# Optimization experiments

Measured on AMD Instinct MI355X. Metric: run time of the kernel, lower is better.

Reference implementation:

```python
import jax, jax.numpy as jnp
import numpy as np

N_NODES = 50000
N_EDGES = 800000
HIDDEN = 128


def setup_inputs() -> dict:
    key = jax.random.key(0)
    k_emb, k_ei, k1, k2, k3, kb1, kb2, kb3 = jax.random.split(key, 8)
    emb = jax.random.normal(k_emb, (N_NODES, HIDDEN), dtype=jnp.float32)
    edge_index = jax.random.randint(k_ei, (2, N_EDGES), 0, N_NODES, dtype=jnp.int64)
    h = HIDDEN
    # MLP([2h, 4h, h, 1]) weights, Kaiming-uniform-ish init
    def lin(k, fan_in, fan_out):
        bound = 1.0 / np.sqrt(fan_in)
        return jax.random.uniform(k, (fan_in, fan_out), jnp.float32, -bound, bound)
    W1 = lin(k1, 2 * h, 4 * h)
    b1 = jax.random.uniform(kb1, (4 * h,), jnp.float32, -1.0 / np.sqrt(2 * h), 1.0 / np.sqrt(2 * h))
    W2 = lin(k2, 4 * h, h)
    b2 = jax.random.uniform(kb2, (h,), jnp.float32, -1.0 / np.sqrt(4 * h), 1.0 / np.sqrt(4 * h))
    W3 = lin(k3, h, 1)
    b3 = jax.random.uniform(kb3, (1,), jnp.float32, -1.0 / np.sqrt(h), 1.0 / np.sqrt(h))
    return {"emb": emb, "edge_index": edge_index,
            "W1": W1, "b1": b1, "W2": W2, "b2": b2, "W3": W3, "b3": b3}


def reference(emb, edge_index, W1, b1, W2, b2, W3, b3):
    # learn_edge_att=True path: gather endpoints, concat, 3-layer MLP
    col, row = edge_index[0], edge_index[1]
    f12 = jnp.concatenate([emb[col], emb[row]], axis=-1)  # [E, 2h]
    x = jax.nn.relu(f12 @ W1 + b1)                         # [E, 4h]
    x = jax.nn.relu(x @ W2 + b2)                           # [E, h]
    att_log_logits = x @ W3 + b3                           # [E, 1]
    return att_log_logits
```

## Files before the change

kernel.cpp:

```cpp
#include <hip/hip_runtime.h>
#include <hip/hip_bf16.h>
#include <stdint.h>

#define N_EDGES   800000
#define N_NODESC  50000
#define HID       128

typedef __attribute__((ext_vector_type(8))) short bf16x8;
typedef __attribute__((ext_vector_type(4))) float f32x4;
typedef __attribute__((ext_vector_type(4))) unsigned int u32x4;

__device__ __forceinline__ short f2bf(float f) {
    union { float f; uint32_t u; } v; v.f = f;
    uint32_t r = v.u + 0x7FFFu + ((v.u >> 16) & 1u);
    return (short)(r >> 16);
}

__device__ __forceinline__ uint32_t packbf2(float lo, float hi) {
    float2 t; t.x = lo; t.y = hi;
    __hip_bfloat162 h = __float22bfloat162_rn(t);
    uint32_t u;
    __builtin_memcpy(&u, &h, 4);
    return u;
}

__device__ __forceinline__ uint32_t addrelu2(uint32_t a, uint32_t b) {
    __hip_bfloat162 ha, hb;
    __builtin_memcpy(&ha, &a, 4);
    __builtin_memcpy(&hb, &b, 4);
    __hip_bfloat162 s = __hadd2(ha, hb);
    uint32_t x;
    __builtin_memcpy(&x, &s, 4);
    uint32_t neg = (x & 0x80008000u) >> 15;
    return x & ~(neg * 0xFFFFu);
}
__device__ __forceinline__ bf16x8 addrelu8(u32x4 p, u32x4 q) {
    u32x4 r;
    #pragma unroll
    for (int j = 0; j < 4; ++j) r[j] = addrelu2(p[j], q[j]);
    bf16x8 out;
    __builtin_memcpy(&out, &r, 16);
    return out;
}

#define PQ_OFF   0UL
#define W1S_OFF  102400000UL
#define W2S_OFF  (W1S_OFF + 262144UL)

__global__ __launch_bounds__(256) void swizzle_kernel(const float* __restrict__ W1,
                                                      const float* __restrict__ W2,
                                                      short* __restrict__ W1s,
                                                      short* __restrict__ W2s) {
    int t = blockIdx.x * 256 + threadIdx.x;
    int lane = t & 63;
    int kq = lane >> 4;
    int nn = lane & 15;
    if (t < 16384) {
        int frag = t >> 6;
        int kc = frag >> 6;
        int nt = frag & 63;
        int n = nt * 16 + nn;
        int kbase = kc * 32 + kq * 8;
        bf16x8 v;
        #pragma unroll
        for (int j = 0; j < 8; ++j) {
            int k = kbase + j;
            float f = (n < 512) ? W1[k * 512 + n] : W1[(128 + k) * 512 + (n - 512)];
            v[j] = f2bf(f);
        }
        *(bf16x8*)(W1s + frag * 512 + lane * 8) = v;
    } else if (t < 24576) {
        int t2 = t - 16384;
        int frag = t2 >> 6;
        int kc = frag >> 3;
        int nt = frag & 7;
        int n = nt * 16 + nn;
        int kbase = kc * 32 + kq * 8;
        bf16x8 v;
        #pragma unroll
        for (int j = 0; j < 8; ++j) v[j] = f2bf(W2[(kbase + j) * HID + n]);
        *(bf16x8*)(W2s + frag * 512 + lane * 8) = v;
    }
}

__global__ __launch_bounds__(256) void precompute_kernel(const float* __restrict__ emb,
                                                         const short* __restrict__ W1s,
                                                         const float* __restrict__ b1,
                                                         short* __restrict__ PQ) {
    int lane = threadIdx.x & 63;
    int w = threadIdx.x >> 6;
    int nb = blockIdx.x * 32;
    int m = lane & 15;
    int kq = lane >> 4;

    int n0 = nb + m;       if (n0 > N_NODESC - 1) n0 = N_NODESC - 1;
    int n1 = nb + 16 + m;  if (n1 > N_NODESC - 1) n1 = N_NODESC - 1;
    const float* a0p = emb + (size_t)n0 * 128 + kq * 8;
    const float* a1p = emb + (size_t)n1 * 128 + kq * 8;

    f32x4 acc[2][16];
    #pragma unroll
    for (int mt = 0; mt < 2; ++mt)
        #pragma unroll
        for (int i = 0; i < 16; ++i) acc[mt][i] = (f32x4){0.f, 0.f, 0.f, 0.f};

    #pragma unroll
    for (int kc = 0; kc < 4; ++kc) {
        f32x4 x0 = *(const f32x4*)(a0p + kc * 32);
        f32x4 x1 = *(const f32x4*)(a0p + kc * 32 + 4);
        f32x4 y0 = *(const f32x4*)(a1p + kc * 32);
        f32x4 y1 = *(const f32x4*)(a1p + kc * 32 + 4);
        u32x4 au, bu;
        au[0] = packbf2(x0[0], x0[1]); au[1] = packbf2(x0[2], x0[3]);
        au[2] = packbf2(x1[0], x1[1]); au[3] = packbf2(x1[2], x1[3]);
        bu[0] = packbf2(y0[0], y0[1]); bu[1] = packbf2(y0[2], y0[3]);
        bu[2] = packbf2(y1[0], y1[1]); bu[3] = packbf2(y1[2], y1[3]);
        bf16x8 a0, a1;
        __builtin_memcpy(&a0, &au, 16);
        __builtin_memcpy(&a1, &bu, 16);
        #pragma unroll
        for (int nt = 0; nt < 16; ++nt) {
            int frag = kc * 64 + (w * 16 + nt);
            bf16x8 b = *(const bf16x8*)(W1s + frag * 512 + lane * 8);
            acc[0][nt] = __builtin_amdgcn_mfma_f32_16x16x32_bf16(a0, b, acc[0][nt], 0, 0, 0);
            acc[1][nt] = __builtin_amdgcn_mfma_f32_16x16x32_bf16(a1, b, acc[1][nt], 0, 0, 0);
        }
    }

    #pragma unroll
    for (int nt = 0; nt < 16; ++nt) {
        int n = w * 256 + nt * 16 + m;
        float bias = (n < 512) ? b1[n] : 0.0f;
        #pragma unroll
        for (int mt = 0; mt < 2; ++mt) {
            #pragma unroll
            for (int r = 0; r < 4; ++r) {
                int node = nb + mt * 16 + kq * 4 + r;
                if (node < N_NODESC)
                    PQ[(size_t)node * 1024 + n] = f2bf(acc[mt][nt][r] + bias);
            }
        }
    }
}

__global__ __launch_bounds__(256, 2) void edge_kernel(const short* __restrict__ PQ,
                                                      const int* __restrict__ ei,
                                                      const short* __restrict__ W2s,
                                                      const float* __restrict__ b2,
                                                      const float* __restrict__ W3,
                                                      const float* __restrict__ b3,
                                                      float* __restrict__ out) {
    int lane = threadIdx.x & 63;
    int w = threadIdx.x >> 6;
    int e0 = blockIdx.x * 256 + w * 64;
    int m = lane & 15;
    int kq = lane >> 4;

    int idx_c = ei[e0 + lane];
    int idx_r = ei[N_EDGES + e0 + lane];

    const short* pb[4];
    const short* qb[4];
    #pragma unroll
    for (int t = 0; t < 4; ++t) {
        int ce = __shfl(idx_c, t * 16 + m, 64);
        int re = __shfl(idx_r, t * 16 + m, 64);
        pb[t] = PQ + (size_t)ce * 1024 + kq * 8;
        qb[t] = PQ + (size_t)re * 1024 + 512 + kq * 8;
    }

    f32x4 acc[4][8];
    #pragma unroll
    for (int t = 0; t < 4; ++t)
        #pragma unroll
        for (int nt = 0; nt < 8; ++nt) acc[t][nt] = (f32x4){0.f, 0.f, 0.f, 0.f};

    #pragma unroll
    for (int kc = 0; kc < 16; ++kc) {
        u32x4 p[4], q[4];
        #pragma unroll
        for (int t = 0; t < 4; ++t) {
            p[t] = *(const u32x4*)(pb[t] + kc * 32);
            q[t] = *(const u32x4*)(qb[t] + kc * 32);
        }
        bf16x8 b[8];
        #pragma unroll
        for (int nt = 0; nt < 8; ++nt)
            b[nt] = *(const bf16x8*)(W2s + (kc * 8 + nt) * 512 + lane * 8);
        #pragma unroll
        for (int t = 0; t < 4; ++t) {
            bf16x8 a = addrelu8(p[t], q[t]);
            #pragma unroll
            for (int nt = 0; nt < 8; ++nt)
                acc[t][nt] = __builtin_amdgcn_mfma_f32_16x16x32_bf16(a, b[nt], acc[t][nt], 0, 0, 0);
        }
    }

    float b2v[8], w3v[8];
    #pragma unroll
    for (int nt = 0; nt < 8; ++nt) {
        b2v[nt] = b2[nt * 16 + m];
        w3v[nt] = W3[nt * 16 + m];
    }
    float b3s = b3[0];
    #pragma unroll
    for (int t = 0; t < 4; ++t) {
        float partial[4] = {0.f, 0.f, 0.f, 0.f};
        #pragma unroll
        for (int nt = 0; nt < 8; ++nt) {
            #pragma unroll
            for (int r = 0; r < 4; ++r) {
                float x2 = acc[t][nt][r] + b2v[nt];
                x2 = x2 > 0.f ? x2 : 0.f;
                partial[r] += x2 * w3v[nt];
            }
        }
        #pragma unroll
        for (int r = 0; r < 4; ++r) {
            #pragma unroll
            for (int off = 1; off < 16; off <<= 1)
                partial[r] += __shfl_xor(partial[r], off, 64);
            if (m == 0) out[e0 + t * 16 + kq * 4 + r] = partial[r] + b3s;
        }
    }
}

extern "C" void kernel_launch(void* const* d_in, const int* in_sizes, int n_in,
                              void* d_out, int out_size, void* d_ws, size_t ws_size,
                              hipStream_t stream) {
    const float* emb = (const float*)d_in[0];
    const int*   ei  = (const int*)d_in[1];
    const float* W1  = (const float*)d_in[2];
    const float* b1  = (const float*)d_in[3];
    const float* W2  = (const float*)d_in[4];
    const float* b2  = (const float*)d_in[5];
    const float* W3  = (const float*)d_in[6];
    const float* b3  = (const float*)d_in[7];
    float* out = (float*)d_out;

    short* PQ  = (short*)((char*)d_ws + PQ_OFF);
    short* W1s = (short*)((char*)d_ws + W1S_OFF);
    short* W2s = (short*)((char*)d_ws + W2S_OFF);

    swizzle_kernel<<<96, 256, 0, stream>>>(W1, W2, W1s, W2s);
    precompute_kernel<<<(N_NODESC + 31) / 32, 256, 0, stream>>>(emb, W1s, b1, PQ);
    edge_kernel<<<N_EDGES / 256, 256, 0, stream>>>(PQ, ei, W2s, b2, W3, b3, out);
}
```

Measured before the change: 475.5 us.

## Counting-sort edges by source node and coalesce precompute stores via LDS

Adds a histogram, scan and scatter pass that sorts edges by their first endpoint, so the edge kernel reads PQ rows with better cache locality and writes outputs through a permutation index. The precompute kernel now stages results in shared memory and writes 16-byte coalesced rows instead of scattered 2-byte stores. The cost is four extra launches, atomics, a single-block serial scan, and scattered output writes.

Measured after the change: 555.5 us. +16.8%, slower.

```diff
diff --git a/kernel.cpp b/kernel.cpp
--- a/kernel.cpp
+++ b/kernel.cpp
@@ -43,9 +43,14 @@
     return out;
 }
 
-#define PQ_OFF   0UL
-#define W1S_OFF  102400000UL
-#define W2S_OFF  (W1S_OFF + 262144UL)
+#define PQ_OFF    0UL
+#define W1S_OFF   102400000UL
+#define W2S_OFF   (W1S_OFF + 262144UL)
+#define CNT_OFF   (W2S_OFF + 131072UL)
+#define CUR_OFF   (CNT_OFF + 200000UL)
+#define COLS_OFF  (CUR_OFF + 200000UL)
+#define ROWS_OFF  (COLS_OFF + 3200000UL)
+#define ES_OFF    (ROWS_OFF + 3200000UL)
 
 __global__ __launch_bounds__(256) void swizzle_kernel(const float* __restrict__ W1,
                                                       const float* __restrict__ W2,
@@ -83,10 +88,48 @@
     }
 }
 
+__global__ __launch_bounds__(256) void hist_kernel(const int* __restrict__ ei,
+                                                   int* __restrict__ cnt) {
+    int e = blockIdx.x * 256 + threadIdx.x;
+    atomicAdd(&cnt[ei[e]], 1);
+}
+
+__global__ __launch_bounds__(1024) void scan_kernel(const int* __restrict__ cnt,
+                                                    int* __restrict__ cursor) {
+    __shared__ int psum[1024];
+    int tid = threadIdx.x;
+    int lo = tid * 49;
+    int hi = lo + 49; if (hi > N_NODESC) hi = N_NODESC;
+    int s = 0;
+    for (int i = lo; i < hi; ++i) s += cnt[i];
+    psum[tid] = s;
+    __syncthreads();
+    if (tid == 0) {
+        int acc = 0;
+        for (int i = 0; i < 1024; ++i) { int t = psum[i]; psum[i] = acc; acc += t; }
+    }
+    __syncthreads();
+    int run = psum[tid];
+    for (int i = lo; i < hi; ++i) { int c = cnt[i]; cursor[i] = run; run += c; }
+}
+
+__global__ __launch_bounds__(256) void scatter_kernel(const int* __restrict__ ei,
+                                                      int* __restrict__ cursor,
+                                                      int* __restrict__ col_s,
+                                                      int* __restrict__ row_s,
+                                                      int* __restrict__ e_s) {
+    int e = blockIdx.x * 256 + threadIdx.x;
+    int c = ei[e];
+    int r = ei[N_EDGES + e];
+    int slot = atomicAdd(&cursor[c], 1);
+    col_s[slot] = c; row_s[slot] = r; e_s[slot] = e;
+}
+
 __global__ __launch_bounds__(256) void precompute_kernel(const float* __restrict__ emb,
                                                          const short* __restrict__ W1s,
                                                          const float* __restrict__ b1,
                                                          short* __restrict__ PQ) {
+    __shared__ short tile[4][16][272];
     int lane = threadIdx.x & 63;
     int w = threadIdx.x >> 6;
     int nb = blockIdx.x * 32;
@@ -128,23 +171,31 @@
     }
 
     #pragma unroll
-    for (int nt = 0; nt < 16; ++nt) {
-        int n = w * 256 + nt * 16 + m;
-        float bias = (n < 512) ? b1[n] : 0.0f;
-        #pragma unroll
-        for (int mt = 0; mt < 2; ++mt) {
+    for (int mt = 0; mt < 2; ++mt) {
+        #pragma unroll
+        for (int nt = 0; nt < 16; ++nt) {
+            int n = w * 256 + nt * 16 + m;
+            float bias = (n < 512) ? b1[n] : 0.0f;
             #pragma unroll
-            for (int r = 0; r < 4; ++r) {
-                int node = nb + mt * 16 + kq * 4 + r;
-                if (node < N_NODESC)
-                    PQ[(size_t)node * 1024 + n] = f2bf(acc[mt][nt][r] + bias);
-            }
+            for (int r = 0; r < 4; ++r)
+                tile[w][kq * 4 + r][nt * 16 + m] = f2bf(acc[mt][nt][r] + bias);
+        }
+        #pragma unroll
+        for (int s = 0; s < 8; ++s) {
+            int row = s * 2 + (lane >> 5);
+            int chunk = lane & 31;
+            int node = nb + mt * 16 + row;
+            bf16x8 v = *(const bf16x8*)(&tile[w][row][chunk * 8]);
+            if (node < N_NODESC)
+                *(bf16x8*)(PQ + (size_t)node * 1024 + w * 256 + chunk * 8) = v;
         }
     }
 }
 
 __global__ __launch_bounds__(256, 2) void edge_kernel(const short* __restrict__ PQ,
-                                                      const int* __restrict__ ei,
+                                                      const int* __restrict__ col_s,
+                                                      const int* __restrict__ row_s,
+                                                      const int* __restrict__ e_s,
                                                       const short* __restrict__ W2s,
                                                       const float* __restrict__ b2,
                                                       const float* __restrict__ W3,
@@ -156,8 +207,8 @@
     int m = lane & 15;
     int kq = lane >> 4;
 
-    int idx_c = ei[e0 + lane];
-    int idx_r = ei[N_EDGES + e0 + lane];
+    int idx_c = col_s[e0 + lane];
+    int idx_r = row_s[e0 + lane];
 
     const short* pb[4];
     const short* qb[4];
@@ -196,6 +247,7 @@
         }
     }
 
+    int eid = e_s[e0 + lane];
     float b2v[8], w3v[8];
     #pragma unroll
     for (int nt = 0; nt < 8; ++nt) {
@@ -220,7 +272,8 @@
             #pragma unroll
             for (int off = 1; off < 16; off <<= 1)
                 partial[r] += __shfl_xor(partial[r], off, 64);
-            if (m == 0) out[e0 + t * 16 + kq * 4 + r] = partial[r] + b3s;
+            int eo = __shfl(eid, t * 16 + kq * 4 + r, 64);
+            if (m == 0) out[eo] = partial[r] + b3s;
         }
     }
 }
@@ -238,11 +291,21 @@
     const float* b3  = (const float*)d_in[7];
     float* out = (float*)d_out;
 
-    short* PQ  = (short*)((char*)d_ws + PQ_OFF);
-    short* W1s = (short*)((char*)d_ws + W1S_OFF);
-    short* W2s = (short*)((char*)d_ws + W2S_OFF);
-
+    short* PQ    = (short*)((char*)d_ws + PQ_OFF);
+    short* W1s   = (short*)((char*)d_ws + W1S_OFF);
+    short* W2s   = (short*)((char*)d_ws + W2S_OFF);
+    int*   cnt   = (int*)((char*)d_ws + CNT_OFF);
+    int*   cur   = (int*)((char*)d_ws + CUR_OFF);
+    int*   col_s = (int*)((char*)d_ws + COLS_OFF);
+    int*   row_s = (int*)((char*)d_ws + ROWS_OFF);
+    int*   e_s   = (int*)((char*)d_ws + ES_OFF);
+
+    hipMemsetAsync(cnt, 0, N_NODESC * sizeof(int), stream);
     swizzle_kernel<<<96, 256, 0, stream>>>(W1, W2, W1s, W2s);
+    hist_kernel<<<N_EDGES / 256, 256, 0, stream>>>(ei, cnt);
+    scan_kernel<<<1, 1024, 0, stream>>>(cnt, cur);
+    scatter_kernel<<<N_EDGES / 256, 256, 0, stream>>>(ei, cur, col_s, row_s, e_s);
     precompute_kernel<<<(N_NODESC + 31) / 32, 256, 0, stream>>>(emb, W1s, b1, PQ);
-    edge_kernel<<<N_EDGES / 256, 256, 0, stream>>>(PQ, ei, W2s, b2, W3, b3, out);
-}
+    edge_kernel<<<N_EDGES / 256, 256, 0, stream>>>(PQ, col_s, row_s, e_s,
+                                                   W2s, b2, W3, b3, out);
+}
```
